# Kernel tuning notes

Hardware: AMD Instinct MI355X
Metric: run time of the kernel (lower is better)

The kernel has to match this reference:

```python
import jax, jax.numpy as jnp
import numpy as np


def hard_sigmoid(x):
    # Keras hard_sigmoid: clip(0.2*x + 0.5, 0, 1)
    return jnp.clip(0.2 * x + 0.5, 0.0, 1.0)


def setup_inputs() -> dict:
    key = jax.random.key(0)
    k1, k2, k3, k4, k5 = jax.random.split(key, 5)
    B, D, U = 8192, 1024, 1024
    return {
        "inputs": jax.random.normal(k1, (B, D), dtype=jnp.float32),
        "h_tm1": jax.random.normal(k2, (B, U), dtype=jnp.float32),
        "kernel": jax.random.normal(k3, (D, 3 * U), dtype=jnp.float32) * 0.02,
        "recurrent_kernel": jax.random.normal(k4, (U, 3 * U), dtype=jnp.float32) * 0.02,
        "bias": jax.random.normal(k5, (2, 3 * U), dtype=jnp.float32) * 0.02,
    }


def reference(inputs, h_tm1, kernel, recurrent_kernel, bias):
    units = recurrent_kernel.shape[0]
    input_bias, recurrent_bias = bias[0], bias[1]

    # [B, 3U] input projection
    matrix_x = inputs @ kernel + input_bias
    x_z, x_r, x_h = jnp.split(matrix_x, 3, axis=-1)

    # [B, 3U] recurrent projection
    matrix_inner = h_tm1 @ recurrent_kernel + recurrent_bias
    rec_z = matrix_inner[:, :units]
    rec_r = matrix_inner[:, units:2 * units]
    rec_h = matrix_inner[:, 2 * units:]

    z = hard_sigmoid(x_z + rec_z)
    r = hard_sigmoid(x_r + rec_r)
    hh = jnp.tanh(x_h + r * rec_h)
    h = z * h_tm1 + (1.0 - z) * hh
    return h
```

## Files before the change

kernel.cpp:

```cpp
#include <hip/hip_runtime.h>
#include <math.h>

typedef __attribute__((ext_vector_type(4))) float floatx4;
typedef __attribute__((ext_vector_type(8))) short shortx8;

#define M_TILE 128
#define N_TILE 64
#define BK 32

__device__ __forceinline__ unsigned short f2bf(float f) {
    union { float f; unsigned int u; } v; v.f = f;
    unsigned int r = v.u + 0x7fffu + ((v.u >> 16) & 1u);
    return (unsigned short)(r >> 16);
}

__device__ __forceinline__ void gload_lds16(const unsigned short* g, unsigned short* l) {
    __builtin_amdgcn_global_load_lds(
        (const __attribute__((address_space(1))) void*)g,
        (__attribute__((address_space(3))) void*)l, 16, 0, 0);
}

__global__ void cvt_kernel(const float* __restrict__ src, unsigned short* __restrict__ dst, int n4) {
    int i = blockIdx.x * blockDim.x + threadIdx.x;
    if (i >= n4) return;
    float4 v = ((const float4*)src)[i];
    ushort4 s;
    s.x = f2bf(v.x); s.y = f2bf(v.y); s.z = f2bf(v.z); s.w = f2bf(v.w);
    ((ushort4*)dst)[i] = s;
}

__global__ void transpose_cvt_kernel(const float* __restrict__ src, unsigned short* __restrict__ dst) {
    __shared__ float t[32][33];
    const int nt = blockIdx.x;
    const int kt = blockIdx.y;
    const int tx = threadIdx.x;
    const int ty = threadIdx.y;
    #pragma unroll
    for (int i = 0; i < 4; ++i) {
        int k = kt * 32 + ty + i * 8;
        t[ty + i * 8][tx] = src[(size_t)k * 3072 + nt * 32 + tx];
    }
    __syncthreads();
    #pragma unroll
    for (int i = 0; i < 4; ++i) {
        int n = nt * 32 + ty + i * 8;
        dst[(size_t)n * 1024 + kt * 32 + tx] = f2bf(t[tx][ty + i * 8]);
    }
}

__global__ __launch_bounds__(256, 2)
void gru_mfma_kernel(const unsigned short* __restrict__ Xb,
                     const unsigned short* __restrict__ Hb,
                     const unsigned short* __restrict__ Wt,
                     const unsigned short* __restrict__ Rt,
                     const float* __restrict__ H,
                     const float* __restrict__ bias,
                     float* __restrict__ out)
{
    __shared__ __attribute__((aligned(16))) unsigned short ldsA[2][M_TILE * BK];
    __shared__ __attribute__((aligned(16))) unsigned short ldsW[6][N_TILE * BK];

    const int tid  = threadIdx.x;
    const int bid  = blockIdx.x;
    const int bn   = bid & 15;
    const int bm   = bid >> 4;
    const int m0   = bm * M_TILE;
    const int n0   = bn * N_TILE;

    const int wid  = tid >> 6;
    const int lane = tid & 63;
    const int wr   = wid >> 1;
    const int wc   = wid & 1;
    const int lo   = lane & 15;
    const int quad = lane >> 4;

    const int srow = lane >> 2;
    const int skof = (lane & 3) * 8;

    floatx4 acc_z[4][2]  = {};
    floatx4 acc_r[4][2]  = {};
    floatx4 acc_xh[4][2] = {};
    floatx4 acc_rh[4][2] = {};

    for (int k0 = 0; k0 < 1024; k0 += BK) {
        #pragma unroll
        for (int r = 0; r < 2; ++r) {
            const int seg = r * 4 + wid;
            const size_t gofs = (size_t)(m0 + seg * 16 + srow) * 1024 + k0 + skof;
            gload_lds16(Xb + gofs, &ldsA[0][seg * 512]);
            gload_lds16(Hb + gofs, &ldsA[1][seg * 512]);
        }
        #pragma unroll
        for (int g = 0; g < 6; ++g) {
            const unsigned short* base = (g < 3) ? Wt : Rt;
            const int gm = (g < 3) ? g : g - 3;
            const size_t gofs = (size_t)(gm * 1024 + n0 + wid * 16 + srow) * 1024 + k0 + skof;
            gload_lds16(base + gofs, &ldsW[g][wid * 512]);
        }
        __syncthreads();

        shortx8 a_in[4], a_h[4];
        #pragma unroll
        for (int i = 0; i < 4; ++i) {
            a_in[i] = *(const shortx8*)&ldsA[0][(wr * 64 + i * 16 + lo) * BK + quad * 8];
            a_h[i]  = *(const shortx8*)&ldsA[1][(wr * 64 + i * 16 + lo) * BK + quad * 8];
        }
        #pragma unroll
        for (int j = 0; j < 2; ++j) {
            const int nc = (wc * 32 + j * 16 + lo) * BK + quad * 8;
            shortx8 bz  = *(const shortx8*)&ldsW[0][nc];
            shortx8 bre = *(const shortx8*)&ldsW[1][nc];
            shortx8 bh  = *(const shortx8*)&ldsW[2][nc];
            shortx8 rz  = *(const shortx8*)&ldsW[3][nc];
            shortx8 rre = *(const shortx8*)&ldsW[4][nc];
            shortx8 rh  = *(const shortx8*)&ldsW[5][nc];
            #pragma unroll
            for (int i = 0; i < 4; ++i) {
                acc_z[i][j]  = __builtin_amdgcn_mfma_f32_16x16x32_bf16(a_in[i], bz,  acc_z[i][j],  0, 0, 0);
                acc_z[i][j]  = __builtin_amdgcn_mfma_f32_16x16x32_bf16(a_h[i],  rz,  acc_z[i][j],  0, 0, 0);
                acc_r[i][j]  = __builtin_amdgcn_mfma_f32_16x16x32_bf16(a_in[i], bre, acc_r[i][j],  0, 0, 0);
                acc_r[i][j]  = __builtin_amdgcn_mfma_f32_16x16x32_bf16(a_h[i],  rre, acc_r[i][j],  0, 0, 0);
                acc_xh[i][j] = __builtin_amdgcn_mfma_f32_16x16x32_bf16(a_in[i], bh,  acc_xh[i][j], 0, 0, 0);
                acc_rh[i][j] = __builtin_amdgcn_mfma_f32_16x16x32_bf16(a_h[i],  rh,  acc_rh[i][j], 0, 0, 0);
            }
        }
        __syncthreads();
    }

    #pragma unroll
    for (int j = 0; j < 2; ++j) {
        const int col = n0 + wc * 32 + j * 16 + lo;
        const float bz  = bias[col]        + bias[3072 + col];
        const float brr = bias[1024 + col] + bias[4096 + col];
        const float b0h = bias[2048 + col];
        const float b1h = bias[5120 + col];
        #pragma unroll
        for (int i = 0; i < 4; ++i) {
            const int rowb = m0 + wr * 64 + i * 16 + quad * 4;
            #pragma unroll
            for (int r = 0; r < 4; ++r) {
                const int row = rowb + r;
                float sz = acc_z[i][j][r]  + bz;
                float sr = acc_r[i][j][r]  + brr;
                float xh = acc_xh[i][j][r] + b0h;
                float rh = acc_rh[i][j][r] + b1h;
                float z   = fminf(fmaxf(0.2f * sz + 0.5f, 0.0f), 1.0f);
                float rr2 = fminf(fmaxf(0.2f * sr + 0.5f, 0.0f), 1.0f);
                float pre = xh + rr2 * rh;
                float e   = __expf(2.0f * pre);
                float th  = 1.0f - 2.0f / (e + 1.0f);
                float hp  = H[(size_t)row * 1024 + col];
                out[(size_t)row * 1024 + col] = z * hp + (1.0f - z) * th;
            }
        }
    }
}

#define KP 40
__global__ __launch_bounds__(256, 2)
void gru_fused_kernel(const float* __restrict__ X, const float* __restrict__ H,
                      const float* __restrict__ W, const float* __restrict__ R,
                      const float* __restrict__ bias, float* __restrict__ out)
{
    __shared__ __attribute__((aligned(16))) unsigned short ldsA[2][M_TILE * KP];
    __shared__ __attribute__((aligned(16))) unsigned short ldsW[6][N_TILE * KP];
    const int tid = threadIdx.x, bid = blockIdx.x;
    const int bn = bid & 15, bm = bid >> 4;
    const int m0 = bm * M_TILE, n0 = bn * N_TILE;
    const int wid = tid >> 6, lane = tid & 63;
    const int wr = wid >> 1, wc = wid & 1;
    const int lo = lane & 15, quad = lane >> 4;
    floatx4 acc_z[4][2] = {}, acc_r[4][2] = {}, acc_xh[4][2] = {}, acc_rh[4][2] = {};
    for (int k0 = 0; k0 < 1024; k0 += BK) {
        #pragma unroll
        for (int i = 0; i < 8; ++i) {
            int idx = tid + i * 256;
            const float* base = (idx < 1024) ? X : H;
            int rem = idx & 1023, row = rem >> 3, kq = rem & 7;
            const float4 v = *(const float4*)(base + (size_t)(m0 + row) * 1024 + k0 + kq * 4);
            ushort4 s; s.x = f2bf(v.x); s.y = f2bf(v.y); s.z = f2bf(v.z); s.w = f2bf(v.w);
            *(ushort4*)&ldsA[idx >> 10][row * KP + kq * 4] = s;
        }
        #pragma unroll
        for (int i = 0; i < 3; ++i) {
            int b = tid + i * 256, g = b >> 7, rem = b & 127, kb = rem >> 4, c4 = rem & 15;
            const float* wb = (g < 3) ? W : R;
            int gm = (g < 3) ? g : g - 3;
            const float* src = wb + (size_t)(k0 + kb * 4) * 3072 + gm * 1024 + n0 + c4 * 4;
            float4 r0 = *(const float4*)(src);
            float4 r1 = *(const float4*)(src + 3072);
            float4 r2 = *(const float4*)(src + 2 * 3072);
            float4 r3 = *(const float4*)(src + 3 * 3072);
            ushort4 s0, s1, s2, s3;
            s0.x=f2bf(r0.x); s0.y=f2bf(r1.x); s0.z=f2bf(r2.x); s0.w=f2bf(r3.x);
            s1.x=f2bf(r0.y); s1.y=f2bf(r1.y); s1.z=f2bf(r2.y); s1.w=f2bf(r3.y);
            s2.x=f2bf(r0.z); s2.y=f2bf(r1.z); s2.z=f2bf(r2.z); s2.w=f2bf(r3.z);
            s3.x=f2bf(r0.w); s3.y=f2bf(r1.w); s3.z=f2bf(r2.w); s3.w=f2bf(r3.w);
            unsigned short* dst = &ldsW[g][0];
            *(ushort4*)&dst[(c4*4+0)*KP + kb*4] = s0;
            *(ushort4*)&dst[(c4*4+1)*KP + kb*4] = s1;
            *(ushort4*)&dst[(c4*4+2)*KP + kb*4] = s2;
            *(ushort4*)&dst[(c4*4+3)*KP + kb*4] = s3;
        }
        __syncthreads();
        shortx8 a_in[4], a_h[4];
        #pragma unroll
        for (int i = 0; i < 4; ++i) {
            a_in[i] = *(const shortx8*)&ldsA[0][(wr*64 + i*16 + lo) * KP + quad*8];
            a_h[i]  = *(const shortx8*)&ldsA[1][(wr*64 + i*16 + lo) * KP + quad*8];
        }
        #pragma unroll
        for (int j = 0; j < 2; ++j) {
            const int nc = (wc*32 + j*16 + lo) * KP + quad*8;
            shortx8 bz  = *(const shortx8*)&ldsW[0][nc];
            shortx8 bre = *(const shortx8*)&ldsW[1][nc];
            shortx8 bh  = *(const shortx8*)&ldsW[2][nc];
            shortx8 rz  = *(const shortx8*)&ldsW[3][nc];
            shortx8 rre = *(const shortx8*)&ldsW[4][nc];
            shortx8 rh  = *(const shortx8*)&ldsW[5][nc];
            #pragma unroll
            for (int i = 0; i < 4; ++i) {
                acc_z[i][j]  = __builtin_amdgcn_mfma_f32_16x16x32_bf16(a_in[i], bz,  acc_z[i][j],  0, 0, 0);
                acc_z[i][j]  = __builtin_amdgcn_mfma_f32_16x16x32_bf16(a_h[i],  rz,  acc_z[i][j],  0, 0, 0);
                acc_r[i][j]  = __builtin_amdgcn_mfma_f32_16x16x32_bf16(a_in[i], bre, acc_r[i][j],  0, 0, 0);
                acc_r[i][j]  = __builtin_amdgcn_mfma_f32_16x16x32_bf16(a_h[i],  rre, acc_r[i][j],  0, 0, 0);
                acc_xh[i][j] = __builtin_amdgcn_mfma_f32_16x16x32_bf16(a_in[i], bh,  acc_xh[i][j], 0, 0, 0);
                acc_rh[i][j] = __builtin_amdgcn_mfma_f32_16x16x32_bf16(a_h[i],  rh,  acc_rh[i][j], 0, 0, 0);
            }
        }
        __syncthreads();
    }
    #pragma unroll
    for (int j = 0; j < 2; ++j) {
        const int col = n0 + wc*32 + j*16 + lo;
        const float bz  = bias[col]        + bias[3072 + col];
        const float brr = bias[1024 + col] + bias[4096 + col];
        const float b0h = bias[2048 + col];
        const float b1h = bias[5120 + col];
        #pragma unroll
        for (int i = 0; i < 4; ++i) {
            const int rowb = m0 + wr*64 + i*16 + quad*4;
            #pragma unroll
            for (int r = 0; r < 4; ++r) {
                const int row = rowb + r;
                float sz = acc_z[i][j][r]  + bz;
                float sr = acc_r[i][j][r]  + brr;
                float xh = acc_xh[i][j][r] + b0h;
                float rh = acc_rh[i][j][r] + b1h;
                float z   = fminf(fmaxf(0.2f * sz + 0.5f, 0.0f), 1.0f);
                float rr2 = fminf(fmaxf(0.2f * sr + 0.5f, 0.0f), 1.0f);
                float pre = xh + rr2 * rh;
                float e   = __expf(2.0f * pre);
                float th  = 1.0f - 2.0f / (e + 1.0f);
                float hp  = H[(size_t)row * 1024 + col];
                out[(size_t)row * 1024 + col] = z * hp + (1.0f - z) * th;
            }
        }
    }
}

extern "C" void kernel_launch(void* const* d_in, const int* in_sizes, int n_in,
                              void* d_out, int out_size, void* d_ws, size_t ws_size,
                              hipStream_t stream)
{
    const float* X    = (const float*)d_in[0];
    const float* H    = (const float*)d_in[1];
    const float* W    = (const float*)d_in[2];
    const float* R    = (const float*)d_in[3];
    const float* bias = (const float*)d_in[4];
    float* out = (float*)d_out;

    const size_t need = (size_t)(8192 * 1024) * 2 * 2 + (size_t)(3072 * 1024) * 2 * 2;
    if (ws_size >= need) {
        unsigned short* Xb = (unsigned short*)d_ws;
        unsigned short* Hb = Xb + (size_t)8192 * 1024;
        unsigned short* Wt = Hb + (size_t)8192 * 1024;
        unsigned short* Rt = Wt + (size_t)3072 * 1024;
        hipLaunchKernelGGL(cvt_kernel, dim3(8192), dim3(256), 0, stream, X, Xb, 2097152);
        hipLaunchKernelGGL(cvt_kernel, dim3(8192), dim3(256), 0, stream, H, Hb, 2097152);
        hipLaunchKernelGGL(transpose_cvt_kernel, dim3(96, 32), dim3(32, 8), 0, stream, W, Wt);
        hipLaunchKernelGGL(transpose_cvt_kernel, dim3(96, 32), dim3(32, 8), 0, stream, R, Rt);
        hipLaunchKernelGGL(gru_mfma_kernel, dim3(1024), dim3(256), 0, stream,
                           Xb, Hb, Wt, Rt, H, bias, out);
    } else {
        hipLaunchKernelGGL(gru_fused_kernel, dim3(1024), dim3(256), 0, stream, X, H, W, R, bias, out);
    }
}
```

Baseline: 247.7 us.

## Double K tile to 64 and merge conversion kernels into one prep launch

Raises the MFMA kernel's K step from 32 to 64, which halves the main-loop iterations and barrier pairs, and reworks the global-to-LDS load mapping to match. The four conversion and transpose kernels are merged into a single prep kernel with 64x64 transpose tiles and vectorized bf16 stores, removing launch overhead. The larger tile doubles LDS use per block (about 80KB), which may cut occupancy below the two blocks per CU the launch bounds assume. The LDS layout keeps rows unpadded, so bank conflicts on fragment reads may rise.

```diff
diff --git a/kernel.cpp b/kernel.cpp
--- a/kernel.cpp
+++ b/kernel.cpp
@@ -6,45 +6,64 @@
 
 #define M_TILE 128
 #define N_TILE 64
-#define BK 32
+#define BK 64
 
 __device__ __forceinline__ unsigned short f2bf(float f) {
     union { float f; unsigned int u; } v; v.f = f;
     unsigned int r = v.u + 0x7fffu + ((v.u >> 16) & 1u);
     return (unsigned short)(r >> 16);
 }
-
 __device__ __forceinline__ void gload_lds16(const unsigned short* g, unsigned short* l) {
     __builtin_amdgcn_global_load_lds(
         (const __attribute__((address_space(1))) void*)g,
         (__attribute__((address_space(3))) void*)l, 16, 0, 0);
 }
 
-__global__ void cvt_kernel(const float* __restrict__ src, unsigned short* __restrict__ dst, int n4) {
-    int i = blockIdx.x * blockDim.x + threadIdx.x;
-    if (i >= n4) return;
-    float4 v = ((const float4*)src)[i];
-    ushort4 s;
-    s.x = f2bf(v.x); s.y = f2bf(v.y); s.z = f2bf(v.z); s.w = f2bf(v.w);
-    ((ushort4*)dst)[i] = s;
-}
-
-__global__ void transpose_cvt_kernel(const float* __restrict__ src, unsigned short* __restrict__ dst) {
-    __shared__ float t[32][33];
-    const int nt = blockIdx.x;
-    const int kt = blockIdx.y;
-    const int tx = threadIdx.x;
-    const int ty = threadIdx.y;
+__global__ void prep_kernel(const float* __restrict__ X, const float* __restrict__ H,
+                            const float* __restrict__ W, const float* __restrict__ R,
+                            unsigned short* __restrict__ Xb, unsigned short* __restrict__ Hb,
+                            unsigned short* __restrict__ Wt, unsigned short* __restrict__ Rt)
+{
+    const int bid = blockIdx.x;
+    const int tx  = threadIdx.x;
+    if (bid < 16384) {
+        const float* src = (bid < 8192) ? X : H;
+        unsigned short* dst = (bid < 8192) ? Xb : Hb;
+        const int i = (bid & 8191) * 256 + tx;
+        float4 v = ((const float4*)src)[i];
+        ushort4 s;
+        s.x = f2bf(v.x); s.y = f2bf(v.y); s.z = f2bf(v.z); s.w = f2bf(v.w);
+        ((ushort4*)dst)[i] = s;
+        return;
+    }
+    __shared__ float tile[64][66];
+    const int tb = bid - 16384;
+    const float* src = (tb < 768) ? W : R;
+    unsigned short* dst = (tb < 768) ? Wt : Rt;
+    const int tt = (tb < 768) ? tb : tb - 768;
+    const int col0 = (tt % 48) * 64;
+    const int k0   = (tt / 48) * 64;
+    const int n4 = tx & 15, kl = tx >> 4;
     #pragma unroll
     for (int i = 0; i < 4; ++i) {
-        int k = kt * 32 + ty + i * 8;
-        t[ty + i * 8][tx] = src[(size_t)k * 3072 + nt * 32 + tx];
+        const int k = kl + i * 16;
+        float4 v = *(const float4*)(src + (size_t)(k0 + k) * 3072 + col0 + n4 * 4);
+        tile[k][n4 * 4 + 0] = v.x; tile[k][n4 * 4 + 1] = v.y;
+        tile[k][n4 * 4 + 2] = v.z; tile[k][n4 * 4 + 3] = v.w;
     }
     __syncthreads();
     #pragma unroll
-    for (int i = 0; i < 4; ++i) {
-        int n = nt * 32 + ty + i * 8;
-        dst[(size_t)n * 1024 + kt * 32 + tx] = f2bf(t[tx][ty + i * 8]);
+    for (int i = 0; i < 2; ++i) {
+        const int c  = tx + i * 256;
+        const int nl = c >> 3, kc = c & 7;
+        ushort4 s0, s1;
+        s0.x = f2bf(tile[kc*8+0][nl]); s0.y = f2bf(tile[kc*8+1][nl]);
+        s0.z = f2bf(tile[kc*8+2][nl]); s0.w = f2bf(tile[kc*8+3][nl]);
+        s1.x = f2bf(tile[kc*8+4][nl]); s1.y = f2bf(tile[kc*8+5][nl]);
+        s1.z = f2bf(tile[kc*8+6][nl]); s1.w = f2bf(tile[kc*8+7][nl]);
+        unsigned short* p = dst + (size_t)(col0 + nl) * 1024 + k0 + kc * 8;
+        *(ushort4*)p = s0;
+        *(ushort4*)(p + 4) = s1;
     }
 }
 
@@ -74,8 +93,8 @@
     const int lo   = lane & 15;
     const int quad = lane >> 4;
 
-    const int srow = lane >> 2;
-    const int skof = (lane & 3) * 8;
+    const int srow = lane >> 3;
+    const int skof = (lane & 7) * 8;
 
     floatx4 acc_z[4][2]  = {};
     floatx4 acc_r[4][2]  = {};
@@ -84,44 +103,53 @@
 
     for (int k0 = 0; k0 < 1024; k0 += BK) {
         #pragma unroll
-        for (int r = 0; r < 2; ++r) {
+        for (int r = 0; r < 8; ++r) {
             const int seg = r * 4 + wid;
-            const size_t gofs = (size_t)(m0 + seg * 16 + srow) * 1024 + k0 + skof;
-            gload_lds16(Xb + gofs, &ldsA[0][seg * 512]);
-            gload_lds16(Hb + gofs, &ldsA[1][seg * 512]);
-        }
-        #pragma unroll
-        for (int g = 0; g < 6; ++g) {
+            const int arr = seg >> 4;
+            const int s   = seg & 15;
+            const size_t gofs = (size_t)(m0 + s * 8 + srow) * 1024 + k0 + skof;
+            gload_lds16(((arr == 0) ? Xb : Hb) + gofs, &ldsA[arr][s * 512]);
+        }
+        #pragma unroll
+        for (int r = 0; r < 12; ++r) {
+            const int seg = r * 4 + wid;
+            const int g   = seg >> 3;
+            const int s   = seg & 7;
             const unsigned short* base = (g < 3) ? Wt : Rt;
             const int gm = (g < 3) ? g : g - 3;
-            const size_t gofs = (size_t)(gm * 1024 + n0 + wid * 16 + srow) * 1024 + k0 + skof;
-            gload_lds16(base + gofs, &ldsW[g][wid * 512]);
+            const size_t gofs = (size_t)(gm * 1024 + n0 + s * 8 + srow) * 1024 + k0 + skof;
+            gload_lds16(base + gofs, &ldsW[g][s * 512]);
         }
         __syncthreads();
 
-        shortx8 a_in[4], a_h[4];
-        #pragma unroll
-        for (int i = 0; i < 4; ++i) {
-            a_in[i] = *(const shortx8*)&ldsA[0][(wr * 64 + i * 16 + lo) * BK + quad * 8];
-            a_h[i]  = *(const shortx8*)&ldsA[1][(wr * 64 + i * 16 + lo) * BK + quad * 8];
-        }
-        #pragma unroll
-        for (int j = 0; j < 2; ++j) {
-            const int nc = (wc * 32 + j * 16 + lo) * BK + quad * 8;
-            shortx8 bz  = *(const shortx8*)&ldsW[0][nc];
-            shortx8 bre = *(const shortx8*)&ldsW[1][nc];
-            shortx8 bh  = *(const shortx8*)&ldsW[2][nc];
-            shortx8 rz  = *(const shortx8*)&ldsW[3][nc];
-            shortx8 rre = *(const shortx8*)&ldsW[4][nc];
-            shortx8 rh  = *(const shortx8*)&ldsW[5][nc];
+        #pragma unroll
+        for (int ks = 0; ks < 2; ++ks) {
+            const int kcp = (ks * 4 + quad) * 8;
+            shortx8 a_in[4], a_h[4];
             #pragma unroll
             for (int i = 0; i < 4; ++i) {
-                acc_z[i][j]  = __builtin_amdgcn_mfma_f32_16x16x32_bf16(a_in[i], bz,  acc_z[i][j],  0, 0, 0);
-                acc_z[i][j]  = __builtin_amdgcn_mfma_f32_16x16x32_bf16(a_h[i],  rz,  acc_z[i][j],  0, 0, 0);
-                acc_r[i][j]  = __builtin_amdgcn_mfma_f32_16x16x32_bf16(a_in[i], bre, acc_r[i][j],  0, 0, 0);
-                acc_r[i][j]  = __builtin_amdgcn_mfma_f32_16x16x32_bf16(a_h[i],  rre, acc_r[i][j],  0, 0, 0);
-                acc_xh[i][j] = __builtin_amdgcn_mfma_f32_16x16x32_bf16(a_in[i], bh,  acc_xh[i][j], 0, 0, 0);
-                acc_rh[i][j] = __builtin_amdgcn_mfma_f32_16x16x32_bf16(a_h[i],  rh,  acc_rh[i][j], 0, 0, 0);
+                const int row = wr * 64 + i * 16 + lo;
+                a_in[i] = *(const shortx8*)&ldsA[0][row * BK + kcp];
+                a_h[i]  = *(const shortx8*)&ldsA[1][row * BK + kcp];
+            }
+            #pragma unroll
+            for (int j = 0; j < 2; ++j) {
+                const int nc = (wc * 32 + j * 16 + lo) * BK + kcp;
+                shortx8 bz  = *(const shortx8*)&ldsW[0][nc];
+                shortx8 bre = *(const shortx8*)&ldsW[1][nc];
+                shortx8 bh  = *(const shortx8*)&ldsW[2][nc];
+                shortx8 rz  = *(const shortx8*)&ldsW[3][nc];
+                shortx8 rre = *(const shortx8*)&ldsW[4][nc];
+                shortx8 rh  = *(const shortx8*)&ldsW[5][nc];
+                #pragma unroll
+                for (int i = 0; i < 4; ++i) {
+                    acc_z[i][j]  = __builtin_amdgcn_mfma_f32_16x16x32_bf16(a_in[i], bz,  acc_z[i][j],  0, 0, 0);
+                    acc_z[i][j]  = __builtin_amdgcn_mfma_f32_16x16x32_bf16(a_h[i],  rz,  acc_z[i][j],  0, 0, 0);
+                    acc_r[i][j]  = __builtin_amdgcn_mfma_f32_16x16x32_bf16(a_in[i], bre, acc_r[i][j],  0, 0, 0);
+                    acc_r[i][j]  = __builtin_amdgcn_mfma_f32_16x16x32_bf16(a_h[i],  rre, acc_r[i][j],  0, 0, 0);
+                    acc_xh[i][j] = __builtin_amdgcn_mfma_f32_16x16x32_bf16(a_in[i], bh,  acc_xh[i][j], 0, 0, 0);
+                    acc_rh[i][j] = __builtin_amdgcn_mfma_f32_16x16x32_bf16(a_h[i],  rh,  acc_rh[i][j], 0, 0, 0);
+                }
             }
         }
         __syncthreads();
@@ -157,6 +185,7 @@
 }
 
 #define KP 40
+#define FBK 32
 __global__ __launch_bounds__(256, 2)
 void gru_fused_kernel(const float* __restrict__ X, const float* __restrict__ H,
                       const float* __restrict__ W, const float* __restrict__ R,
@@ -171,7 +200,7 @@
     const int wr = wid >> 1, wc = wid & 1;
     const int lo = lane & 15, quad = lane >> 4;
     floatx4 acc_z[4][2] = {}, acc_r[4][2] = {}, acc_xh[4][2] = {}, acc_rh[4][2] = {};
-    for (int k0 = 0; k0 < 1024; k0 += BK) {
+    for (int k0 = 0; k0 < 1024; k0 += FBK) {
         #pragma unroll
         for (int i = 0; i < 8; ++i) {
             int idx = tid + i * 256;
@@ -276,10 +305,8 @@
         unsigned short* Hb = Xb + (size_t)8192 * 1024;
         unsigned short* Wt = Hb + (size_t)8192 * 1024;
         unsigned short* Rt = Wt + (size_t)3072 * 1024;
-        hipLaunchKernelGGL(cvt_kernel, dim3(8192), dim3(256), 0, stream, X, Xb, 2097152);
-        hipLaunchKernelGGL(cvt_kernel, dim3(8192), dim3(256), 0, stream, H, Hb, 2097152);
-        hipLaunchKernelGGL(transpose_cvt_kernel, dim3(96, 32), dim3(32, 8), 0, stream, W, Wt);
-        hipLaunchKernelGGL(transpose_cvt_kernel, dim3(96, 32), dim3(32, 8), 0, stream, R, Rt);
+        hipLaunchKernelGGL(prep_kernel, dim3(16384 + 1536), dim3(256), 0, stream,
+                           X, H, W, R, Xb, Hb, Wt, Rt);
         hipLaunchKernelGGL(gru_mfma_kernel, dim3(1024), dim3(256), 0, stream,
                            Xb, Hb, Wt, Rt, H, bias, out);
     } else {
```

Measured after the change: 237.8 us. 1.04x faster.
